# Kernel optimization log

Hardware: AMD Instinct MI355X
Metric: run time of the kernel (lower is better)

The kernel has to match this reference:

```python
import jax, jax.numpy as jnp
import numpy as np

B, K, V, N, M, TOPK = 256, 256, 256, 4000, 4000, 8
EPS = 1e-8  # torch F.cosine_similarity default eps


def setup_inputs() -> dict:
    key = jax.random.key(0)
    ks = jax.random.split(key, 6)
    query_key = jax.random.normal(ks[0], (B, K), dtype=jnp.float32)
    W_k = jax.random.normal(ks[1], (K, K), dtype=jnp.float32) / np.sqrt(K).astype(np.float32)
    b_k = jnp.zeros((K,), dtype=jnp.float32)
    assoc_matrix = jax.random.normal(ks[2], (N, K, V), dtype=jnp.float32) * 0.02
    usage_counter = jax.random.uniform(ks[3], (N,), dtype=jnp.float32) * 10.0
    memory_index = jax.random.randint(ks[4], (M,), 0, N)
    return {
        "query_key": query_key,
        "W_k": W_k,
        "b_k": b_k,
        "assoc_matrix": assoc_matrix,
        "usage_counter": usage_counter,
        "memory_index": memory_index,
        "top_k": TOPK,
    }


def reference(query_key, W_k, b_k, assoc_matrix, usage_counter, memory_index, top_k):
    # key_encoder: Linear + Tanh
    e = jnp.tanh(query_key @ W_k.T + b_k)                      # [B, K]
    # stored keys = first value-column of each used slot (irregular gather)
    stored_keys = assoc_matrix[memory_index, :, 0]             # [M, K]
    # cosine similarity (vectorized form of the per-slot python loop)
    qn = e / jnp.maximum(jnp.linalg.norm(e, axis=-1, keepdims=True), EPS)
    kn = stored_keys / jnp.maximum(jnp.linalg.norm(stored_keys, axis=-1, keepdims=True), EPS)
    sims = qn @ kn.T                                           # [B, M]
    top_sims, top_idx = jax.lax.top_k(sims, top_k)             # [B, k]
    actual = memory_index[top_idx]                             # [B, k] slot ids
    # confidence = sim * (1 + log(1 + usage))
    confidences = top_sims * (1.0 + jnp.log1p(usage_counter[actual]))
    # gather stored associations and retrieve values: e @ A[actual]
    gathered = assoc_matrix[actual]                            # [B, k, K, V]
    retrieved_values = jnp.einsum('bd,bkdv->bkv', e, gathered) # [B, k, V]
    return retrieved_values, confidences, top_sims
```

## Files before the change

kernel.cpp:

```cpp
#include <hip/hip_runtime.h>
#include <math.h>

#define BB 256
#define KK 256
#define VV 256
#define MM 4000
#define TOPK 8

__global__ void k_proj(const float* __restrict__ qk, const float* __restrict__ Wk,
                       const float* __restrict__ bk, double* __restrict__ e64,
                       double* __restrict__ qn64) {
    int b = blockIdx.x, j = threadIdx.x;
    __shared__ float q[KK];
    __shared__ double red[256];
    q[j] = qk[b * KK + j];
    __syncthreads();
    const float* w = Wk + (size_t)j * KK;
    double acc = 0.0;
#pragma unroll 4
    for (int d = 0; d < KK; ++d) acc += (double)q[d] * (double)w[d];
    double val = tanh(acc + (double)bk[j]);
    e64[b * KK + j] = val;
    red[j] = val * val;
    __syncthreads();
    for (int s = 128; s > 0; s >>= 1) {
        if (j < s) red[j] += red[j + s];
        __syncthreads();
    }
    double nrm = fmax(sqrt(red[0]), 1e-8);
    qn64[b * KK + j] = val / nrm;
}

__global__ void k_kn(const float* __restrict__ A, const int* __restrict__ midx,
                     double* __restrict__ kn64) {
    int m = blockIdx.x, t = threadIdx.x;
    size_t n = (size_t)midx[m];
    double val = (double)A[n * (size_t)(KK * VV) + (size_t)t * VV];
    __shared__ double red[256];
    red[t] = val * val;
    __syncthreads();
    for (int s = 128; s > 0; s >>= 1) {
        if (t < s) red[t] += red[t + s];
        __syncthreads();
    }
    double nrm = fmax(sqrt(red[0]), 1e-8);
    kn64[(size_t)m * KK + t] = val / nrm;
}

#define BMS 32
#define BNS 64
#define KS  16
__global__ void __launch_bounds__(128) k_sims(
        const double* __restrict__ qn, const double* __restrict__ kn,
        double* __restrict__ sims) {
    __shared__ double qsT[KS][BMS + 2];
    __shared__ double ksT[KS][BNS + 2];
    int tid = threadIdx.x;
    int tx = tid & 15;
    int ty = tid >> 4;
    int m0 = blockIdx.x * BNS;
    int b0 = blockIdx.y * BMS;
    double acc[4][4] = {};
    int qr = tid >> 2;
    int qc = (tid & 3) * 4;
    int kr = tid >> 1;
    int kc = (tid & 1) * 8;
    bool kval = (m0 + kr) < MM;
    const double* qrow = qn + (size_t)(b0 + qr) * KK;
    const double* krow = kn + (size_t)(m0 + (kval ? kr : 0)) * KK;
    for (int kk = 0; kk < KK; kk += KS) {
#pragma unroll
        for (int j = 0; j < 4; ++j)
            qsT[qc + j][qr] = qrow[kk + qc + j];
#pragma unroll
        for (int j = 0; j < 8; ++j)
            ksT[kc + j][kr] = kval ? krow[kk + kc + j] : 0.0;
        __syncthreads();
#pragma unroll
        for (int i = 0; i < KS; ++i) {
            double qv[4], kv[4];
            *(double2*)&qv[0] = *(const double2*)&qsT[i][ty * 4];
            *(double2*)&qv[2] = *(const double2*)&qsT[i][ty * 4 + 2];
            *(double2*)&kv[0] = *(const double2*)&ksT[i][tx * 4];
            *(double2*)&kv[2] = *(const double2*)&ksT[i][tx * 4 + 2];
#pragma unroll
            for (int a = 0; a < 4; ++a)
#pragma unroll
                for (int c = 0; c < 4; ++c)
                    acc[a][c] += qv[a] * kv[c];
        }
        __syncthreads();
    }
#pragma unroll
    for (int a = 0; a < 4; ++a) {
        int bb = b0 + ty * 4 + a;
#pragma unroll
        for (int c = 0; c < 4; ++c) {
            int mm2 = m0 + tx * 4 + c;
            if (mm2 < MM) sims[(size_t)bb * MM + mm2] = acc[a][c];
        }
    }
}

__global__ void k_topk(const double* __restrict__ sims, const int* __restrict__ midx,
                       const float* __restrict__ usage, float* __restrict__ out_conf,
                       float* __restrict__ out_sims, int* __restrict__ acts) {
    int b = blockIdx.x, t = threadIdx.x;
    double v[TOPK];
    int id[TOPK];
#pragma unroll
    for (int i = 0; i < TOPK; ++i) { v[i] = -INFINITY; id[i] = 0x7fffffff; }
    const double* row = sims + (size_t)b * MM;
    for (int m = t; m < MM; m += 256) {
        double x = row[m];
        if (x > v[TOPK - 1]) {
            v[TOPK - 1] = x; id[TOPK - 1] = m;
#pragma unroll
            for (int i = TOPK - 1; i > 0; --i) {
                if (v[i] > v[i - 1]) {
                    double tv = v[i]; v[i] = v[i - 1]; v[i - 1] = tv;
                    int ti = id[i]; id[i] = id[i - 1]; id[i - 1] = ti;
                }
            }
        }
    }
    __shared__ double sv[256 * TOPK];
    __shared__ int si[256 * TOPK];
#pragma unroll
    for (int i = 0; i < TOPK; ++i) { sv[t * TOPK + i] = v[i]; si[t * TOPK + i] = id[i]; }
    __syncthreads();
    for (int stride = 128; stride > 0; stride >>= 1) {
        if (t < stride) {
            double* av = &sv[t * TOPK];
            int*    ai = &si[t * TOPK];
            double* bv = &sv[(t + stride) * TOPK];
            int*    bi = &si[(t + stride) * TOPK];
            double mv[TOPK]; int mi[TOPK];
            int pa = 0, pb = 0;
#pragma unroll
            for (int i = 0; i < TOPK; ++i) {
                double va = av[pa], vb = bv[pb];
                bool takeA = (va > vb) || (va == vb && ai[pa] < bi[pb]);
                if (takeA) { mv[i] = va; mi[i] = ai[pa]; ++pa; }
                else       { mv[i] = vb; mi[i] = bi[pb]; ++pb; }
            }
#pragma unroll
            for (int i = 0; i < TOPK; ++i) { av[i] = mv[i]; ai[i] = mi[i]; }
        }
        __syncthreads();
    }
    if (t < TOPK) {
        double val = sv[t];
        int idx = si[t];
        int actual = midx[idx];
        out_sims[b * TOPK + t] = (float)val;
        out_conf[b * TOPK + t] = (float)(val * (1.0 + log1p((double)usage[actual])));
        acts[b * TOPK + t] = actual;
    }
}

__global__ void __launch_bounds__(256) k_retr(
        const float* __restrict__ A, const double* __restrict__ e64,
        const int* __restrict__ acts, float* __restrict__ out) {
    int bk_ = blockIdx.x;
    int b = bk_ >> 3;
    int tid = threadIdx.x;
    int w = tid >> 6, l = tid & 63;
    size_t n = (size_t)acts[bk_];
    const float* Ap = A + n * (size_t)(KK * VV);
    __shared__ float es[KK];
    __shared__ float part[4][64][4];
    es[tid] = (float)e64[b * KK + tid];
    __syncthreads();
    float ax = 0.f, ay = 0.f, az = 0.f, aw = 0.f;
    const float* base = Ap + (size_t)(w * 64) * VV + 4 * l;
#pragma unroll 8
    for (int dd = 0; dd < 64; ++dd) {
        float ev = es[w * 64 + dd];
        const float4 a = *reinterpret_cast<const float4*>(base + (size_t)dd * VV);
        ax = fmaf(ev, a.x, ax); ay = fmaf(ev, a.y, ay);
        az = fmaf(ev, a.z, az); aw = fmaf(ev, a.w, aw);
    }
    part[w][l][0] = ax; part[w][l][1] = ay; part[w][l][2] = az; part[w][l][3] = aw;
    __syncthreads();
    int l2 = tid >> 2, j = tid & 3;
    float s = part[0][l2][j] + part[1][l2][j] + part[2][l2][j] + part[3][l2][j];
    out[(size_t)bk_ * VV + tid] = s;
}

extern "C" void kernel_launch(void* const* d_in, const int* in_sizes, int n_in,
                              void* d_out, int out_size, void* d_ws, size_t ws_size,
                              hipStream_t stream) {
    const float* qk    = (const float*)d_in[0];
    const float* Wk    = (const float*)d_in[1];
    const float* bk    = (const float*)d_in[2];
    const float* A     = (const float*)d_in[3];
    const float* usage = (const float*)d_in[4];
    const int*   midx  = (const int*)d_in[5];

    float* out   = (float*)d_out;
    float* retr  = out;
    float* conf  = out + (size_t)BB * TOPK * VV;
    float* tsims = conf + BB * TOPK;

    double* ws64  = (double*)d_ws;
    double* e64   = ws64;
    double* qn64  = e64 + BB * KK;
    double* kn64  = qn64 + BB * KK;
    double* sims  = kn64 + (size_t)MM * KK;
    int*    acts  = (int*)(sims + (size_t)BB * MM);

    k_proj<<<BB, 256, 0, stream>>>(qk, Wk, bk, e64, qn64);
    k_kn<<<MM, 256, 0, stream>>>(A, midx, kn64);
    dim3 g3((MM + BNS - 1) / BNS, BB / BMS);
    k_sims<<<g3, 128, 0, stream>>>(qn64, kn64, sims);
    k_topk<<<BB, 256, 0, stream>>>(sims, midx, usage, conf, tsims, acts);
    k_retr<<<BB * TOPK, 256, 0, stream>>>(A, e64, acts, retr);
}
```

Before: 178.6 us.

## Double-buffer the FP64 similarity GEMM with register prefetch and smaller tiles

The similarity GEMM now uses two shared-memory buffers and loads the next K-slice into registers while computing on the current one, so each step needs one barrier instead of two. The block tile shrinks to 16x64 with 64 threads, which doubles the grid. The K tile is loaded with double2 vector loads and stored with a padded column layout meant to reduce LDS bank conflicts. In exchange the kernel uses more registers and shared memory, and each block reuses less data.

Measured after the change: 174.3 us. 2.4% less time.

```diff
diff --git a/kernel.cpp b/kernel.cpp
--- a/kernel.cpp
+++ b/kernel.cpp
@@ -47,47 +47,86 @@
     kn64[(size_t)m * KK + t] = val / nrm;
 }
 
-#define BMS 32
+#define BMS 16
 #define BNS 64
 #define KS  16
-__global__ void __launch_bounds__(128) k_sims(
+__global__ void __launch_bounds__(64) k_sims(
         const double* __restrict__ qn, const double* __restrict__ kn,
         double* __restrict__ sims) {
-    __shared__ double qsT[KS][BMS + 2];
-    __shared__ double ksT[KS][BNS + 2];
+    __shared__ double qsT[2][KS][BMS + 2];
+    __shared__ double ksT[2][KS][BNS + 8];
     int tid = threadIdx.x;
-    int tx = tid & 15;
-    int ty = tid >> 4;
-    int m0 = blockIdx.x * BNS;
-    int b0 = blockIdx.y * BMS;
+    int tx = tid & 15, ty = tid >> 4;
+    int m0 = blockIdx.x * BNS, b0 = blockIdx.y * BMS;
+    int qr = tid & 15;
+    int qc = (tid >> 4) * 4;
+    int krr = tid >> 3;
+    int kc = (tid & 7) * 2;
+    const double* qrow = qn + (size_t)(b0 + qr) * KK;
     double acc[4][4] = {};
-    int qr = tid >> 2;
-    int qc = (tid & 3) * 4;
-    int kr = tid >> 1;
-    int kc = (tid & 1) * 8;
-    bool kval = (m0 + kr) < MM;
-    const double* qrow = qn + (size_t)(b0 + qr) * KK;
-    const double* krow = kn + (size_t)(m0 + (kval ? kr : 0)) * KK;
-    for (int kk = 0; kk < KK; kk += KS) {
-#pragma unroll
-        for (int j = 0; j < 4; ++j)
-            qsT[qc + j][qr] = qrow[kk + qc + j];
-#pragma unroll
-        for (int j = 0; j < 8; ++j)
-            ksT[kc + j][kr] = kval ? krow[kk + kc + j] : 0.0;
-        __syncthreads();
+    int pb = tx * 4 + (tx >> 2) * 2;
+
+    {
+        double qreg[4]; double2 kreg[8]; int rr[8];
+#pragma unroll
+        for (int j = 0; j < 4; ++j) qreg[j] = qrow[qc + j];
+#pragma unroll
+        for (int s = 0; s < 8; ++s) {
+            int r = krr + s * 8; rr[s] = r;
+            int mrow = m0 + r;
+            const double* kp = kn + (size_t)(mrow < MM ? mrow : 0) * KK + kc;
+            kreg[s] = (mrow < MM) ? *(const double2*)kp : make_double2(0.0, 0.0);
+        }
+#pragma unroll
+        for (int j = 0; j < 4; ++j) qsT[0][qc + j][qr] = qreg[j];
+#pragma unroll
+        for (int s = 0; s < 8; ++s) {
+            int p = rr[s] + (rr[s] >> 4) * 2;
+            ksT[0][kc][p]     = kreg[s].x;
+            ksT[0][kc + 1][p] = kreg[s].y;
+        }
+    }
+    __syncthreads();
+
+    for (int t = 0; t < KK / KS; ++t) {
+        int cur = t & 1;
+        double qreg[4]; double2 kreg[8]; int rr[8];
+        bool have = (t < KK / KS - 1);
+        if (have) {
+            int kk2 = (t + 1) * KS;
+#pragma unroll
+            for (int j = 0; j < 4; ++j) qreg[j] = qrow[kk2 + qc + j];
+#pragma unroll
+            for (int s = 0; s < 8; ++s) {
+                int r = krr + s * 8; rr[s] = r;
+                int mrow = m0 + r;
+                const double* kp = kn + (size_t)(mrow < MM ? mrow : 0) * KK + kk2 + kc;
+                kreg[s] = (mrow < MM) ? *(const double2*)kp : make_double2(0.0, 0.0);
+            }
+        }
 #pragma unroll
         for (int i = 0; i < KS; ++i) {
             double qv[4], kv[4];
-            *(double2*)&qv[0] = *(const double2*)&qsT[i][ty * 4];
-            *(double2*)&qv[2] = *(const double2*)&qsT[i][ty * 4 + 2];
-            *(double2*)&kv[0] = *(const double2*)&ksT[i][tx * 4];
-            *(double2*)&kv[2] = *(const double2*)&ksT[i][tx * 4 + 2];
+            *(double2*)&qv[0] = *(const double2*)&qsT[cur][i][ty * 4];
+            *(double2*)&qv[2] = *(const double2*)&qsT[cur][i][ty * 4 + 2];
+            *(double2*)&kv[0] = *(const double2*)&ksT[cur][i][pb];
+            *(double2*)&kv[2] = *(const double2*)&ksT[cur][i][pb + 2];
 #pragma unroll
             for (int a = 0; a < 4; ++a)
 #pragma unroll
                 for (int c = 0; c < 4; ++c)
                     acc[a][c] += qv[a] * kv[c];
+        }
+        if (have) {
+            int nxt = cur ^ 1;
+#pragma unroll
+            for (int j = 0; j < 4; ++j) qsT[nxt][qc + j][qr] = qreg[j];
+#pragma unroll
+            for (int s = 0; s < 8; ++s) {
+                int p = rr[s] + (rr[s] >> 4) * 2;
+                ksT[nxt][kc][p]     = kreg[s].x;
+                ksT[nxt][kc + 1][p] = kreg[s].y;
+            }
         }
         __syncthreads();
     }
@@ -213,7 +252,7 @@
     k_proj<<<BB, 256, 0, stream>>>(qk, Wk, bk, e64, qn64);
     k_kn<<<MM, 256, 0, stream>>>(A, midx, kn64);
     dim3 g3((MM + BNS - 1) / BNS, BB / BMS);
-    k_sims<<<g3, 128, 0, stream>>>(qn64, kn64, sims);
+    k_sims<<<g3, 64, 0, stream>>>(qn64, kn64, sims);
     k_topk<<<BB, 256, 0, stream>>>(sims, midx, usage, conf, tsims, acts);
     k_retr<<<BB * TOPK, 256, 0, stream>>>(A, e64, acts, retr);
 }
```
